# Performance work log

Hardware: AMD Instinct MI355X
Metric: run time of the kernel (lower is better)

The kernel has to match this reference:

```python
import jax, jax.numpy as jnp
import numpy as np

BN_EPS = 1e-5


def setup_inputs() -> dict:
    key = jax.random.key(0)
    k1, k2 = jax.random.split(key)
    bs, planes, h, w = 16, 64, 256, 256
    x = jax.random.normal(k1, (bs, planes, h, w), dtype=jnp.float32)
    # kaiming_normal_ on (planes, h, h): fan_in = h*h, std = sqrt(2/fan_in)
    std = np.sqrt(2.0 / (h * h)).astype(np.float32)
    weights = jax.random.normal(k2, (planes, h, h), dtype=jnp.float32) * std
    gamma = jnp.ones((planes,), dtype=jnp.float32)
    beta = jnp.zeros((planes,), dtype=jnp.float32)
    return {"x": x, "weights": weights, "gamma": gamma, "beta": beta}


def reference(x, weights, gamma, beta):
    bs, planes, h, w = x.shape
    xf = x.reshape(bs * planes, h, w)
    # batched Gram matrix: [bs*planes, h, h]
    g = jnp.einsum('nij,nkj->nik', xf, xf)
    g = jnp.triu(g)                              # keep upper triangle (incl. diag)
    g = g.reshape(bs, planes, h, h) * weights[None]  # per-plane elementwise weight
    # BatchNorm2d (training mode): biased batch stats over (N, H, W) per channel
    mean = jnp.mean(g, axis=(0, 2, 3), keepdims=True)
    var = jnp.mean(jnp.square(g - mean), axis=(0, 2, 3), keepdims=True)
    g_hat = (g - mean) * jax.lax.rsqrt(var + BN_EPS)
    out = g_hat * gamma[None, :, None, None] + beta[None, :, None, None]
    return out
```

## Files before the change

kernel.cpp:

```cpp
#include <hip/hip_runtime.h>

#define HD 256
#define NCH 64
#define NB 16
#define NPLANE (NB * NCH)
#define NPC (NB * HD * HD)
#define PLANE_ELEMS (HD * HD)

typedef __attribute__((ext_vector_type(4))) float f32x4;
typedef __attribute__((ext_vector_type(8))) short s16x8;
typedef __attribute__((ext_vector_type(4))) short s16x4;

__device__ __forceinline__ short f2bf(float f) {
    unsigned u = __float_as_uint(f);
    u += 0x7FFFu + ((u >> 16) & 1u);
    return (short)(u >> 16);
}
__device__ __forceinline__ float bf2f(short s) {
    return __uint_as_float(((unsigned)(unsigned short)s) << 16);
}

__device__ __forceinline__ s16x8 ldfrag64(const short* B, int row, int q) {
    return *(const s16x8*)&B[row * 64 + ((q ^ (row & 7)) << 3)];
}

__global__ __launch_bounds__(512, 4) void gram_kernel(
    const float* __restrict__ x, const float* __restrict__ w,
    short* __restrict__ raw, float* __restrict__ stats)
{
    const int tile = blockIdx.x;
    const int ti = (tile == 2) ? 1 : 0;
    const int tk = (tile == 0) ? 0 : 1;
    const bool diag = (ti == tk);
    const int b = blockIdx.y;
    const int c = blockIdx.z;
    const int n = b * NCH + c;
    const int tid = threadIdx.x;
    const int wid = tid >> 6, lane = tid & 63;
    const int waveM = wid >> 2;
    const int waveN = wid & 3;
    const int lrow = lane & 15;
    const int qlane = lane >> 4;

    __shared__ short As[2][8192];
    __shared__ short Bs[2][8192];
    __shared__ float redS[8], redQ[8];

    const float* xpA = x + (size_t)n * PLANE_ELEMS + (size_t)(ti * 128) * HD;
    const float* xpB = x + (size_t)n * PLANE_ELEMS + (size_t)(tk * 128) * HD;

    const int rs = tid >> 3;
    const int qs = tid & 7;

    f32x4 acc[4][2];
    #pragma unroll
    for (int i = 0; i < 4; ++i) {
        acc[i][0] = (f32x4){0.f, 0.f, 0.f, 0.f};
        acc[i][1] = (f32x4){0.f, 0.f, 0.f, 0.f};
    }

    f32x4 lA[2][2], lB[2][2];

    #pragma unroll
    for (int j = 0; j < 2; ++j) {
        const float* pA = xpA + (size_t)(j * 64 + rs) * HD + qs * 8;
        lA[j][0] = *(const f32x4*)pA;
        lA[j][1] = *(const f32x4*)(pA + 4);
        if (!diag) {
            const float* pB = xpB + (size_t)(j * 64 + rs) * HD + qs * 8;
            lB[j][0] = *(const f32x4*)pB;
            lB[j][1] = *(const f32x4*)(pB + 4);
        }
    }
    #pragma unroll
    for (int j = 0; j < 2; ++j) {
        const int row = j * 64 + rs;
        const int off = row * 64 + ((qs ^ (row & 7)) << 3);
        s16x8 oa = { f2bf(lA[j][0].x), f2bf(lA[j][0].y), f2bf(lA[j][0].z), f2bf(lA[j][0].w),
                     f2bf(lA[j][1].x), f2bf(lA[j][1].y), f2bf(lA[j][1].z), f2bf(lA[j][1].w) };
        *(s16x8*)&As[0][off] = oa;
        if (!diag) {
            s16x8 ob = { f2bf(lB[j][0].x), f2bf(lB[j][0].y), f2bf(lB[j][0].z), f2bf(lB[j][0].w),
                         f2bf(lB[j][1].x), f2bf(lB[j][1].y), f2bf(lB[j][1].z), f2bf(lB[j][1].w) };
            *(s16x8*)&Bs[0][off] = ob;
        }
    }

    #pragma unroll
    for (int kc = 0; kc < 4; ++kc) {
        __syncthreads();
        if (kc < 3) {
            #pragma unroll
            for (int j = 0; j < 2; ++j) {
                const float* pA = xpA + (size_t)(j * 64 + rs) * HD + (kc + 1) * 64 + qs * 8;
                lA[j][0] = *(const f32x4*)pA;
                lA[j][1] = *(const f32x4*)(pA + 4);
                if (!diag) {
                    const float* pB = xpB + (size_t)(j * 64 + rs) * HD + (kc + 1) * 64 + qs * 8;
                    lB[j][0] = *(const f32x4*)pB;
                    lB[j][1] = *(const f32x4*)(pB + 4);
                }
            }
        }
        const short* Ab = As[kc & 1];
        const short* Bb = diag ? Ab : Bs[kc & 1];
        #pragma unroll
        for (int kk = 0; kk < 2; ++kk) {
            const int q = kk * 4 + qlane;
            s16x8 af[4], bf[2];
            #pragma unroll
            for (int mi = 0; mi < 4; ++mi)
                af[mi] = ldfrag64(Ab, waveM * 64 + mi * 16 + lrow, q);
            #pragma unroll
            for (int ni = 0; ni < 2; ++ni)
                bf[ni] = ldfrag64(Bb, waveN * 32 + ni * 16 + lrow, q);
            #pragma unroll
            for (int mi = 0; mi < 4; ++mi)
                #pragma unroll
                for (int ni = 0; ni < 2; ++ni)
                    acc[mi][ni] = __builtin_amdgcn_mfma_f32_16x16x32_bf16(
                        af[mi], bf[ni], acc[mi][ni], 0, 0, 0);
        }
        if (kc < 3) {
            #pragma unroll
            for (int j = 0; j < 2; ++j) {
                const int row = j * 64 + rs;
                const int off = row * 64 + ((qs ^ (row & 7)) << 3);
                s16x8 oa = { f2bf(lA[j][0].x), f2bf(lA[j][0].y), f2bf(lA[j][0].z), f2bf(lA[j][0].w),
                             f2bf(lA[j][1].x), f2bf(lA[j][1].y), f2bf(lA[j][1].z), f2bf(lA[j][1].w) };
                *(s16x8*)&As[(kc + 1) & 1][off] = oa;
                if (!diag) {
                    s16x8 ob = { f2bf(lB[j][0].x), f2bf(lB[j][0].y), f2bf(lB[j][0].z), f2bf(lB[j][0].w),
                                 f2bf(lB[j][1].x), f2bf(lB[j][1].y), f2bf(lB[j][1].z), f2bf(lB[j][1].w) };
                    *(s16x8*)&Bs[(kc + 1) & 1][off] = ob;
                }
            }
        }
    }

    const float* wp = w + (size_t)c * PLANE_ELEMS;
    short* rp = raw + (size_t)n * PLANE_ELEMS;
    float lsum = 0.f, lsq = 0.f;
    const int row0 = qlane * 4;
    const int col0 = lrow;
    #pragma unroll
    for (int mi = 0; mi < 4; ++mi) {
        #pragma unroll
        for (int ni = 0; ni < 2; ++ni) {
            const int gk = tk * 128 + waveN * 32 + ni * 16 + col0;
            #pragma unroll
            for (int r = 0; r < 4; ++r) {
                const int gi = ti * 128 + waveM * 64 + mi * 16 + row0 + r;
                const bool keep = diag ? (gk >= gi) : true;
                float v = acc[mi][ni][r];
                float val = keep ? v * wp[gi * HD + gk] : 0.f;
                lsum += val;
                lsq  += val * val;
                rp[gi * HD + gk] = f2bf(val);
            }
        }
    }

    #pragma unroll
    for (int off = 32; off > 0; off >>= 1) {
        lsum += __shfl_down(lsum, off);
        lsq  += __shfl_down(lsq, off);
    }
    if (lane == 0) { redS[wid] = lsum; redQ[wid] = lsq; }
    __syncthreads();
    if (tid == 0) {
        float s = 0.f, s2 = 0.f;
        #pragma unroll
        for (int i = 0; i < 8; ++i) { s += redS[i]; s2 += redQ[i]; }
        atomicAdd(&stats[2 * c],     s);
        atomicAdd(&stats[2 * c + 1], s2);
    }
}

__global__ __launch_bounds__(256) void bn_kernel(
    const float* __restrict__ gamma, const float* __restrict__ beta,
    float* __restrict__ out, const float* __restrict__ stats,
    const short* __restrict__ raw)
{
    const int n   = blockIdx.x;
    const int seg = blockIdx.y;
    const int tid = threadIdx.x;
    const int c   = n & (NCH - 1);

    float s  = stats[2 * c];
    float sq = stats[2 * c + 1];
    float mean = s * (1.0f / (float)NPC);
    float var  = sq * (1.0f / (float)NPC) - mean * mean;
    float rstd = rsqrtf(var + 1e-5f);
    float scale = rstd * gamma[c];
    float shift = beta[c] - mean * scale;

    const short* rp = raw + (size_t)n * PLANE_ELEMS;
    float* op = out + (size_t)n * PLANE_ELEMS;
    f32x4 cv = {shift, shift, shift, shift};

    #pragma unroll
    for (int k = 0; k < 2; ++k) {
        const int idx8 = seg * 512 + k * 256 + tid;
        const int r  = idx8 >> 5;
        const int c8 = idx8 & 31;
        const bool cst = (r < 128) ? ((c8 * 8 + 7) < r)
                                   : (c8 < 16 || (((c8 - 16) * 8 + 7) < (r - 128)));
        float* o = &op[(size_t)idx8 * 8];
        if (cst) {
            *(f32x4*)o       = cv;
            *(f32x4*)(o + 4) = cv;
        } else {
            s16x8 v = *(const s16x8*)&rp[(size_t)idx8 * 8];
            f32x4 lo = { bf2f(v[0]) * scale + shift, bf2f(v[1]) * scale + shift,
                         bf2f(v[2]) * scale + shift, bf2f(v[3]) * scale + shift };
            f32x4 hi = { bf2f(v[4]) * scale + shift, bf2f(v[5]) * scale + shift,
                         bf2f(v[6]) * scale + shift, bf2f(v[7]) * scale + shift };
            *(f32x4*)o       = lo;
            *(f32x4*)(o + 4) = hi;
        }
    }
}

template <int PASS>
__global__ __launch_bounds__(256) void gram_bn_fb(
    const float* __restrict__ x, const float* __restrict__ w,
    const float* __restrict__ gamma, const float* __restrict__ beta,
    float* __restrict__ out, float* __restrict__ stats)
{
    const int tile = blockIdx.x;
    const int b    = blockIdx.y;
    const int c    = blockIdx.z;
    const int n    = b * NCH + c;
    const int tid  = threadIdx.x;

    float mean = 0.f, rstd = 0.f, gm = 0.f, bt = 0.f;
    if (PASS == 1) {
        float s  = stats[2*c];
        float sq = stats[2*c+1];
        mean = s * (1.0f / (float)NPC);
        float var = sq * (1.0f / (float)NPC) - mean * mean;
        rstd = rsqrtf(var + 1e-5f);
        gm = gamma[c]; bt = beta[c];
    }
    if (PASS == 1 && tile == 3) {
        float v = (0.f - mean) * rstd * gm + bt;
        f32x4 vv = {v, v, v, v};
        float* op = out + (size_t)n * PLANE_ELEMS;
        for (int it = 0; it < 16; ++it) {
            int t  = it * 256 + tid;
            int r  = t >> 5;
            int c4 = (t & 31) * 4;
            *(f32x4*)&op[(size_t)(128 + r) * HD + c4] = vv;
        }
        return;
    }
    int ti, tk;
    if      (tile == 0) { ti = 0; tk = 0; }
    else if (tile == 1) { ti = 0; tk = 1; }
    else                { ti = 1; tk = 1; }
    const float* xp = x + (size_t)n * PLANE_ELEMS;
    __shared__ short As[128 * 40];
    __shared__ short Bs[128 * 40];
    __shared__ float red[512];
    const int wid   = tid >> 6;
    const int lane  = tid & 63;
    const int waveM = wid >> 1, waveN = wid & 1;
    const int lrow  = lane & 15;
    const int lkk   = (lane >> 4) * 8;
    f32x4 acc[4][4];
    for (int i = 0; i < 4; ++i)
        for (int j = 0; j < 4; ++j)
            acc[i][j] = (f32x4){0.f, 0.f, 0.f, 0.f};
    const int rr = tid >> 3;
    const int cc = (tid & 7) * 4;
    for (int kb = 0; kb < 8; ++kb) {
        for (int it = 0; it < 4; ++it) {
            int r = rr + it * 32;
            f32x4 av = *(const f32x4*)&xp[(size_t)(ti*128 + r) * HD + kb*32 + cc];
            f32x4 bv = *(const f32x4*)&xp[(size_t)(tk*128 + r) * HD + kb*32 + cc];
            s16x4 a4 = { f2bf(av.x), f2bf(av.y), f2bf(av.z), f2bf(av.w) };
            s16x4 b4 = { f2bf(bv.x), f2bf(bv.y), f2bf(bv.z), f2bf(bv.w) };
            *(s16x4*)&As[r*40 + cc] = a4;
            *(s16x4*)&Bs[r*40 + cc] = b4;
        }
        __syncthreads();
        s16x8 af[4], bfr[4];
        for (int mi = 0; mi < 4; ++mi)
            af[mi]  = *(s16x8*)&As[(waveM*64 + mi*16 + lrow)*40 + lkk];
        for (int ni = 0; ni < 4; ++ni)
            bfr[ni] = *(s16x8*)&Bs[(waveN*64 + ni*16 + lrow)*40 + lkk];
        for (int mi = 0; mi < 4; ++mi)
            for (int ni = 0; ni < 4; ++ni)
                acc[mi][ni] = __builtin_amdgcn_mfma_f32_16x16x32_bf16(
                    af[mi], bfr[ni], acc[mi][ni], 0, 0, 0);
        __syncthreads();
    }
    float lsum = 0.f, lsq = 0.f;
    const int row0 = (lane >> 4) * 4;
    const int col0 = lane & 15;
    for (int mi = 0; mi < 4; ++mi) {
        for (int ni = 0; ni < 4; ++ni) {
            int gk = tk*128 + waveN*64 + ni*16 + col0;
            for (int r = 0; r < 4; ++r) {
                int gi = ti*128 + waveM*64 + mi*16 + row0 + r;
                float v = acc[mi][ni][r];
                float val = (gk >= gi)
                    ? v * w[(size_t)c * PLANE_ELEMS + (size_t)gi * HD + gk]
                    : 0.f;
                if (PASS == 0) { lsum += val; lsq += val * val; }
                else out[(size_t)n * PLANE_ELEMS + (size_t)gi * HD + gk] =
                        (val - mean) * rstd * gm + bt;
            }
        }
    }
    if (PASS == 0) {
        red[tid] = lsum; red[256 + tid] = lsq;
        __syncthreads();
        for (int s = 128; s > 0; s >>= 1) {
            if (tid < s) { red[tid] += red[tid+s]; red[256+tid] += red[256+tid+s]; }
            __syncthreads();
        }
        if (tid == 0) {
            atomicAdd(&stats[2*c],     red[0]);
            atomicAdd(&stats[2*c + 1], red[256]);
        }
    }
}

extern "C" void kernel_launch(void* const* d_in, const int* in_sizes, int n_in,
                              void* d_out, int out_size, void* d_ws, size_t ws_size,
                              hipStream_t stream) {
    const float* x     = (const float*)d_in[0];
    const float* w     = (const float*)d_in[1];
    const float* gamma = (const float*)d_in[2];
    const float* beta  = (const float*)d_in[3];
    float* out   = (float*)d_out;
    float* stats = (float*)d_ws;

    hipMemsetAsync(d_ws, 0, 128 * sizeof(float), stream);

    const size_t raw_bytes = (size_t)NPLANE * PLANE_ELEMS * sizeof(short);
    if (ws_size >= 1024 + raw_bytes) {
        short* raw = (short*)((char*)d_ws + 1024);
        gram_kernel<<<dim3(3, NB, NCH), dim3(512), 0, stream>>>(x, w, raw, stats);
        bn_kernel<<<dim3(NPLANE, 16), dim3(256), 0, stream>>>(gamma, beta, out, stats, raw);
    } else {
        gram_bn_fb<0><<<dim3(3, NB, NCH), dim3(256), 0, stream>>>(x, w, gamma, beta, out, stats);
        gram_bn_fb<1><<<dim3(4, NB, NCH), dim3(256), 0, stream>>>(x, w, gamma, beta, out, stats);
    }
}
```

Baseline: 599.6 us.

## Use 64x64 upper-triangular tiles with XCD-aware block mapping in Gram kernel

Changes the Gram kernel from three 128x128 tiles per plane to ten 64x64 upper-triangle tiles on a flat 1D grid of 256-thread blocks. Block IDs are remapped so that consecutive blocks on each XCD cover the same plane, and global loads are prefetched two k-chunks ahead with a single LDS buffer. This skips more of the masked lower triangle (less MMA work and fewer raw writes), and the BN kernel's constant-fill condition now covers every fully lower-triangular 8-column group. In exchange, blocks are smaller, more x rows are reloaded across tiles, and there are more atomics per channel.

```diff
diff --git a/kernel.cpp b/kernel.cpp
--- a/kernel.cpp
+++ b/kernel.cpp
@@ -23,134 +23,113 @@
 __device__ __forceinline__ s16x8 ldfrag64(const short* B, int row, int q) {
     return *(const s16x8*)&B[row * 64 + ((q ^ (row & 7)) << 3)];
 }
-
-__global__ __launch_bounds__(512, 4) void gram_kernel(
+__device__ __forceinline__ void wr_lds(short* buf, int row, int qs,
+                                       const f32x4& a, const f32x4& b) {
+    s16x8 o = { f2bf(a.x), f2bf(a.y), f2bf(a.z), f2bf(a.w),
+                f2bf(b.x), f2bf(b.y), f2bf(b.z), f2bf(b.w) };
+    *(s16x8*)&buf[row * 64 + ((qs ^ (row & 7)) << 3)] = o;
+}
+
+__global__ __launch_bounds__(256, 4) void gram_kernel(
     const float* __restrict__ x, const float* __restrict__ w,
     short* __restrict__ raw, float* __restrict__ stats)
 {
-    const int tile = blockIdx.x;
-    const int ti = (tile == 2) ? 1 : 0;
-    const int tk = (tile == 0) ? 0 : 1;
-    const bool diag = (ti == tk);
-    const int b = blockIdx.y;
-    const int c = blockIdx.z;
-    const int n = b * NCH + c;
+    const int bid = blockIdx.x;
+    const int wk  = (bid & 7) * 1280 + (bid >> 3);
+    const int plane = wk / 10;
+    const int t = wk - plane * 10;
+    const int I = (t < 4) ? 0 : (t < 7) ? 1 : (t < 9) ? 2 : 3;
+    const int J = t - ((I == 0) ? 0 : (I == 1) ? 4 : (I == 2) ? 7 : 9) + I;
+    const bool diag = (I == J);
+    const int c = plane & (NCH - 1);
     const int tid = threadIdx.x;
     const int wid = tid >> 6, lane = tid & 63;
-    const int waveM = wid >> 2;
-    const int waveN = wid & 3;
-    const int lrow = lane & 15;
-    const int qlane = lane >> 4;
-
-    __shared__ short As[2][8192];
-    __shared__ short Bs[2][8192];
-    __shared__ float redS[8], redQ[8];
-
-    const float* xpA = x + (size_t)n * PLANE_ELEMS + (size_t)(ti * 128) * HD;
-    const float* xpB = x + (size_t)n * PLANE_ELEMS + (size_t)(tk * 128) * HD;
-
-    const int rs = tid >> 3;
+    const int wm = wid >> 1, wn = wid & 1;
+    const int lrow = lane & 15, qlane = lane >> 4;
+
+    __shared__ short As[4096];
+    __shared__ short Bs[4096];
+    __shared__ float redS[4], redQ[4];
+
+    const float* xpA = x + (size_t)plane * PLANE_ELEMS + (size_t)(I * 64) * HD;
+    const float* xpB = x + (size_t)plane * PLANE_ELEMS + (size_t)(J * 64) * HD;
+    const int r0 = tid >> 3;
     const int qs = tid & 7;
 
-    f32x4 acc[4][2];
-    #pragma unroll
-    for (int i = 0; i < 4; ++i) {
-        acc[i][0] = (f32x4){0.f, 0.f, 0.f, 0.f};
-        acc[i][1] = (f32x4){0.f, 0.f, 0.f, 0.f};
-    }
-
-    f32x4 lA[2][2], lB[2][2];
-
-    #pragma unroll
-    for (int j = 0; j < 2; ++j) {
-        const float* pA = xpA + (size_t)(j * 64 + rs) * HD + qs * 8;
-        lA[j][0] = *(const f32x4*)pA;
-        lA[j][1] = *(const f32x4*)(pA + 4);
-        if (!diag) {
-            const float* pB = xpB + (size_t)(j * 64 + rs) * HD + qs * 8;
-            lB[j][0] = *(const f32x4*)pB;
-            lB[j][1] = *(const f32x4*)(pB + 4);
-        }
-    }
-    #pragma unroll
-    for (int j = 0; j < 2; ++j) {
-        const int row = j * 64 + rs;
-        const int off = row * 64 + ((qs ^ (row & 7)) << 3);
-        s16x8 oa = { f2bf(lA[j][0].x), f2bf(lA[j][0].y), f2bf(lA[j][0].z), f2bf(lA[j][0].w),
-                     f2bf(lA[j][1].x), f2bf(lA[j][1].y), f2bf(lA[j][1].z), f2bf(lA[j][1].w) };
-        *(s16x8*)&As[0][off] = oa;
-        if (!diag) {
-            s16x8 ob = { f2bf(lB[j][0].x), f2bf(lB[j][0].y), f2bf(lB[j][0].z), f2bf(lB[j][0].w),
-                         f2bf(lB[j][1].x), f2bf(lB[j][1].y), f2bf(lB[j][1].z), f2bf(lB[j][1].w) };
-            *(s16x8*)&Bs[0][off] = ob;
+    f32x4 acc[2][2];
+    #pragma unroll
+    for (int i = 0; i < 2; ++i)
+        #pragma unroll
+        for (int j = 0; j < 2; ++j)
+            acc[i][j] = (f32x4){0.f, 0.f, 0.f, 0.f};
+
+    f32x4 sA[2][4], sB[2][4];
+
+    #pragma unroll
+    for (int kc = 0; kc < 2; ++kc) {
+        #pragma unroll
+        for (int j = 0; j < 2; ++j) {
+            const float* p = xpA + (size_t)(j * 32 + r0) * HD + kc * 64 + qs * 8;
+            sA[kc][j * 2]     = *(const f32x4*)p;
+            sA[kc][j * 2 + 1] = *(const f32x4*)(p + 4);
+            if (!diag) {
+                const float* pb = xpB + (size_t)(j * 32 + r0) * HD + kc * 64 + qs * 8;
+                sB[kc][j * 2]     = *(const f32x4*)pb;
+                sB[kc][j * 2 + 1] = *(const f32x4*)(pb + 4);
+            }
         }
     }
 
     #pragma unroll
     for (int kc = 0; kc < 4; ++kc) {
-        __syncthreads();
-        if (kc < 3) {
+        const int st = kc & 1;
+        if (kc > 0) __syncthreads();
+        #pragma unroll
+        for (int j = 0; j < 2; ++j) {
+            wr_lds(As, j * 32 + r0, qs, sA[st][j * 2], sA[st][j * 2 + 1]);
+            if (!diag)
+                wr_lds(Bs, j * 32 + r0, qs, sB[st][j * 2], sB[st][j * 2 + 1]);
+        }
+        if (kc < 2) {
             #pragma unroll
             for (int j = 0; j < 2; ++j) {
-                const float* pA = xpA + (size_t)(j * 64 + rs) * HD + (kc + 1) * 64 + qs * 8;
-                lA[j][0] = *(const f32x4*)pA;
-                lA[j][1] = *(const f32x4*)(pA + 4);
+                const float* p = xpA + (size_t)(j * 32 + r0) * HD + (kc + 2) * 64 + qs * 8;
+                sA[st][j * 2]     = *(const f32x4*)p;
+                sA[st][j * 2 + 1] = *(const f32x4*)(p + 4);
                 if (!diag) {
-                    const float* pB = xpB + (size_t)(j * 64 + rs) * HD + (kc + 1) * 64 + qs * 8;
-                    lB[j][0] = *(const f32x4*)pB;
-                    lB[j][1] = *(const f32x4*)(pB + 4);
+                    const float* pb = xpB + (size_t)(j * 32 + r0) * HD + (kc + 2) * 64 + qs * 8;
+                    sB[st][j * 2]     = *(const f32x4*)pb;
+                    sB[st][j * 2 + 1] = *(const f32x4*)(pb + 4);
                 }
             }
         }
-        const short* Ab = As[kc & 1];
-        const short* Bb = diag ? Ab : Bs[kc & 1];
+        __syncthreads();
+        const short* Bsrc = diag ? As : Bs;
         #pragma unroll
         for (int kk = 0; kk < 2; ++kk) {
             const int q = kk * 4 + qlane;
-            s16x8 af[4], bf[2];
-            #pragma unroll
-            for (int mi = 0; mi < 4; ++mi)
-                af[mi] = ldfrag64(Ab, waveM * 64 + mi * 16 + lrow, q);
-            #pragma unroll
-            for (int ni = 0; ni < 2; ++ni)
-                bf[ni] = ldfrag64(Bb, waveN * 32 + ni * 16 + lrow, q);
-            #pragma unroll
-            for (int mi = 0; mi < 4; ++mi)
-                #pragma unroll
-                for (int ni = 0; ni < 2; ++ni)
-                    acc[mi][ni] = __builtin_amdgcn_mfma_f32_16x16x32_bf16(
-                        af[mi], bf[ni], acc[mi][ni], 0, 0, 0);
-        }
-        if (kc < 3) {
-            #pragma unroll
-            for (int j = 0; j < 2; ++j) {
-                const int row = j * 64 + rs;
-                const int off = row * 64 + ((qs ^ (row & 7)) << 3);
-                s16x8 oa = { f2bf(lA[j][0].x), f2bf(lA[j][0].y), f2bf(lA[j][0].z), f2bf(lA[j][0].w),
-                             f2bf(lA[j][1].x), f2bf(lA[j][1].y), f2bf(lA[j][1].z), f2bf(lA[j][1].w) };
-                *(s16x8*)&As[(kc + 1) & 1][off] = oa;
-                if (!diag) {
-                    s16x8 ob = { f2bf(lB[j][0].x), f2bf(lB[j][0].y), f2bf(lB[j][0].z), f2bf(lB[j][0].w),
-                                 f2bf(lB[j][1].x), f2bf(lB[j][1].y), f2bf(lB[j][1].z), f2bf(lB[j][1].w) };
-                    *(s16x8*)&Bs[(kc + 1) & 1][off] = ob;
-                }
-            }
+            s16x8 af0 = ldfrag64(As,   wm * 32 +      lrow, q);
+            s16x8 af1 = ldfrag64(As,   wm * 32 + 16 + lrow, q);
+            s16x8 bf0 = ldfrag64(Bsrc, wn * 32 +      lrow, q);
+            s16x8 bf1 = ldfrag64(Bsrc, wn * 32 + 16 + lrow, q);
+            acc[0][0] = __builtin_amdgcn_mfma_f32_16x16x32_bf16(af0, bf0, acc[0][0], 0, 0, 0);
+            acc[0][1] = __builtin_amdgcn_mfma_f32_16x16x32_bf16(af0, bf1, acc[0][1], 0, 0, 0);
+            acc[1][0] = __builtin_amdgcn_mfma_f32_16x16x32_bf16(af1, bf0, acc[1][0], 0, 0, 0);
+            acc[1][1] = __builtin_amdgcn_mfma_f32_16x16x32_bf16(af1, bf1, acc[1][1], 0, 0, 0);
         }
     }
 
     const float* wp = w + (size_t)c * PLANE_ELEMS;
-    short* rp = raw + (size_t)n * PLANE_ELEMS;
+    short* rp = raw + (size_t)plane * PLANE_ELEMS;
     float lsum = 0.f, lsq = 0.f;
-    const int row0 = qlane * 4;
-    const int col0 = lrow;
-    #pragma unroll
-    for (int mi = 0; mi < 4; ++mi) {
+    #pragma unroll
+    for (int mi = 0; mi < 2; ++mi) {
         #pragma unroll
         for (int ni = 0; ni < 2; ++ni) {
-            const int gk = tk * 128 + waveN * 32 + ni * 16 + col0;
+            const int gk = J * 64 + wn * 32 + ni * 16 + lrow;
             #pragma unroll
             for (int r = 0; r < 4; ++r) {
-                const int gi = ti * 128 + waveM * 64 + mi * 16 + row0 + r;
+                const int gi = I * 64 + wm * 32 + mi * 16 + qlane * 4 + r;
                 const bool keep = diag ? (gk >= gi) : true;
                 float v = acc[mi][ni][r];
                 float val = keep ? v * wp[gi * HD + gk] : 0.f;
@@ -169,9 +148,8 @@
     if (lane == 0) { redS[wid] = lsum; redQ[wid] = lsq; }
     __syncthreads();
     if (tid == 0) {
-        float s = 0.f, s2 = 0.f;
-        #pragma unroll
-        for (int i = 0; i < 8; ++i) { s += redS[i]; s2 += redQ[i]; }
+        float s = redS[0] + redS[1] + redS[2] + redS[3];
+        float s2 = redQ[0] + redQ[1] + redQ[2] + redQ[3];
         atomicAdd(&stats[2 * c],     s);
         atomicAdd(&stats[2 * c + 1], s2);
     }
@@ -204,8 +182,7 @@
         const int idx8 = seg * 512 + k * 256 + tid;
         const int r  = idx8 >> 5;
         const int c8 = idx8 & 31;
-        const bool cst = (r < 128) ? ((c8 * 8 + 7) < r)
-                                   : (c8 < 16 || (((c8 - 16) * 8 + 7) < (r - 128)));
+        const bool cst = (c8 * 8 + 7) < r;
         float* o = &op[(size_t)idx8 * 8];
         if (cst) {
             *(f32x4*)o       = cv;
@@ -343,7 +320,7 @@
     const size_t raw_bytes = (size_t)NPLANE * PLANE_ELEMS * sizeof(short);
     if (ws_size >= 1024 + raw_bytes) {
         short* raw = (short*)((char*)d_ws + 1024);
-        gram_kernel<<<dim3(3, NB, NCH), dim3(512), 0, stream>>>(x, w, raw, stats);
+        gram_kernel<<<dim3(10240), dim3(256), 0, stream>>>(x, w, raw, stats);
         bn_kernel<<<dim3(NPLANE, 16), dim3(256), 0, stream>>>(gamma, beta, out, stats, raw);
     } else {
         gram_bn_fb<0><<<dim3(3, NB, NCH), dim3(256), 0, stream>>>(x, w, gamma, beta, out, stats);
```

Result: no change. 594.9 us (-0.8%).
